# Performance work log

Hardware: AMD Instinct MI355X
Metric: run time of the kernel (lower is better)

## Reference

```python
import jax, jax.numpy as jnp
import numpy as np
import math

B, L = 2048, 60
D, H, NL = 80, 8, 3
HD = D // H            # head_dim = 10
NLOC, NUSR = 1187, 46
DFF = 2 * D
IN_DIM = D + 24 + 32 + 2   # loc(80)+user(24)+weekday(16)+hour(16)+2 continuous


def _ln(x, g, b):
    m = jnp.mean(x, -1, keepdims=True)
    v = jnp.mean((x - m) ** 2, -1, keepdims=True)
    return (x - m) * jax.lax.rsqrt(v + 1e-5) * g + b


def setup_inputs():
    key = jax.random.key(0)
    k = lambda i: jax.random.fold_in(key, i)
    g = lambda i, shp, s: jax.random.normal(k(i), shp, dtype=jnp.float32) * s
    inp = {
        "loc_seq": jax.random.randint(k(0), (B, L), 0, NLOC),
        "user_seq": jax.random.randint(k(1), (B, L), 0, NUSR),
        "weekday_seq": jax.random.randint(k(2), (B, L), 0, 8),
        "start_min_seq": jax.random.randint(k(3), (B, L), 0, 1440),
        "dur_seq": jax.random.randint(k(4), (B, L), 0, 600),
        "diff_seq": jax.random.randint(k(5), (B, L), 0, 100),
        "seq_len": jax.random.randint(k(6), (B,), 1, L + 1),
    }
    # embedding tables (padding_idx=0 rows zeroed where the module uses it)
    inp["loc_table"] = g(10, (NLOC, D), 0.02).at[0].set(0.0)
    inp["user_table"] = g(11, (NUSR, 24), 0.02).at[0].set(0.0)
    inp["wk_table"] = g(12, (8, 16), 0.02).at[0].set(0.0)
    inp["hr_table"] = g(13, (25, 16), 0.02)
    inp["in_w"] = g(14, (IN_DIM, D), 0.09)
    inp["in_b"] = jnp.zeros((D,), jnp.float32)
    inp["in_g"] = jnp.ones((D,), jnp.float32)
    inp["in_be"] = jnp.zeros((D,), jnp.float32)
    inp["pos_emb"] = g(15, (1, L, D), 0.02)
    # per-layer stacked params (NL=3 layers)
    inp["qkv_w"] = g(16, (NL, D, 3 * D), 0.09)
    inp["proj_w"] = g(17, (NL, D, D), 0.11)
    inp["proj_b"] = jnp.zeros((NL, D), jnp.float32)
    inp["rel_emb"] = g(18, (NL, 2 * L - 1, HD), 1.0)
    inp["n1_g"] = jnp.ones((NL, D), jnp.float32)
    inp["n1_b"] = jnp.zeros((NL, D), jnp.float32)
    inp["ffn_w1"] = g(19, (NL, D, DFF), 0.09)
    inp["ffn_b1"] = jnp.zeros((NL, DFF), jnp.float32)
    inp["ffn_w2"] = g(20, (NL, DFF, D), 0.09)
    inp["ffn_b2"] = jnp.zeros((NL, D), jnp.float32)
    inp["n2_g"] = jnp.ones((NL, D), jnp.float32)
    inp["n2_b"] = jnp.zeros((NL, D), jnp.float32)
    inp["fn_g"] = jnp.ones((D,), jnp.float32)
    inp["fn_b"] = jnp.zeros((D,), jnp.float32)
    inp["pr_w1"] = g(21, (D, D), 0.11)
    inp["pr_b1"] = jnp.zeros((D,), jnp.float32)
    inp["pr_w2"] = g(22, (D, NLOC), 0.04)
    inp["pr_b2"] = jnp.zeros((NLOC,), jnp.float32)
    inp["protos"] = g(23, (NLOC, D), 0.04)
    inp["temp"] = jnp.asarray(2.0, jnp.float32)
    return inp


def reference(loc_seq, user_seq, weekday_seq, start_min_seq, dur_seq, diff_seq, seq_len,
              loc_table, user_table, wk_table, hr_table, in_w, in_b, in_g, in_be, pos_emb,
              qkv_w, proj_w, proj_b, rel_emb, n1_g, n1_b, ffn_w1, ffn_b1, ffn_w2, ffn_b2,
              n2_g, n2_b, fn_g, fn_b, pr_w1, pr_b1, pr_w2, pr_b2, protos, temp):
    Bx, Lx = loc_seq.shape
    loc_e = loc_table[loc_seq]                                            # [B,L,80]
    user_e = jnp.broadcast_to(user_table[user_seq[:, 0]][:, None, :], (Bx, Lx, 24))
    hour = jnp.clip(start_min_seq // 60, 0, 23)
    cont = jnp.stack([diff_seq.astype(jnp.float32) / 10.0,
                      dur_seq.astype(jnp.float32) / 300.0], -1)           # [B,L,2]
    x = jnp.concatenate([loc_e, user_e, wk_table[weekday_seq], hr_table[hour], cont], -1)
    x = _ln(x @ in_w + in_b, in_g, in_be) + pos_emb[:, :Lx, :]
    key_mask = loc_seq == 0                                               # mask keys [B,L]
    pos_idx = jnp.arange(Lx)[None, :] - jnp.arange(Lx)[:, None] + (Lx - 1)  # [L,L]
    scale = 1.0 / math.sqrt(HD)
    for l in range(NL):
        qkv = (x @ qkv_w[l]).reshape(Bx, Lx, 3, H, HD)
        q = qkv[:, :, 0].transpose(0, 2, 1, 3)                            # [B,H,L,hd]
        kk = qkv[:, :, 1].transpose(0, 2, 1, 3)
        v = qkv[:, :, 2].transpose(0, 2, 1, 3)
        rel = rel_emb[l][pos_idx]                                         # [L,L,hd]
        attn = (jnp.einsum('bhid,bhjd->bhij', q, kk)
                + jnp.einsum('bhid,ijd->bhij', q, rel)) * scale
        attn = jnp.where(key_mask[:, None, None, :], -jnp.inf, attn)
        a = jax.nn.softmax(attn, -1)
        o = jnp.einsum('bhij,bhjd->bhid', a, v).transpose(0, 2, 1, 3).reshape(Bx, Lx, D)
        x = _ln(x + o @ proj_w[l] + proj_b[l], n1_g[l], n1_b[l])
        f = jax.nn.gelu(x @ ffn_w1[l] + ffn_b1[l], approximate=False) @ ffn_w2[l] + ffn_b2[l]
        x = _ln(x + f, n2_g[l], n2_b[l])
    x = _ln(x, fn_g, fn_b)
    final = x[jnp.arange(Bx), jnp.clip(seq_len - 1, 0, Lx - 1)]           # [B,80]
    logits_param = jax.nn.gelu(final @ pr_w1 + pr_b1, approximate=False) @ pr_w2 + pr_b2
    fnorm = final / jnp.maximum(jnp.linalg.norm(final, axis=-1, keepdims=True), 1e-12)
    pnorm = protos / jnp.maximum(jnp.linalg.norm(protos, axis=-1, keepdims=True), 1e-12)
    logits = 0.5 * logits_param + 0.5 * (fnorm @ pnorm.T) * 15.0
    return logits / jnp.clip(temp, 0.5, 3.0)
```

## Files before the change

kernel.cpp:

```cpp
#include <hip/hip_runtime.h>
#include <hip/hip_bf16.h>
#include <math.h>

#define BB   2048
#define LL   60
#define DD   80
#define HH   8
#define HDD  10
#define NLNUM 3
#define NLOC 1187
#define DFF  160
#define IN_DIM 138
#define RELN 119
#define SCS  68
#define XP   21
#define HP   41
#define VP   35
#define TS   65

__device__ __forceinline__ float gelu_f(float a) {
  float x = fabsf(a) * 0.70710678118654752f;
  float t = 1.0f / (1.0f + 0.3275911f * x);
  float y = t * (0.254829592f + t * (-0.284496736f + t * (1.421413741f +
            t * (-1.453152027f + t * 1.061405429f))));
  float e = 1.0f - y * __expf(-x * x);
  float erf_s = copysignf(e, a);
  return 0.5f * a * (1.0f + erf_s);
}

__global__ __launch_bounds__(256) void k_rprep(
    const float* __restrict__ rel_emb, float* __restrict__ relTg) {
  int idx = blockIdx.x * 256 + threadIdx.x;
  if (idx >= 3600) return;
  int p = idx % 120;
  int d = (idx / 120) % 10;
  int l = idx / 1200;
  float v = 0.0f;
  if (p < RELN) v = rel_emb[l * RELN * HDD + p * HDD + d];
  relTg[idx] = v;
}

__global__ __launch_bounds__(256) void k_embed(
    const int* __restrict__ loc_seq, const int* __restrict__ user_seq,
    const int* __restrict__ wk_seq, const int* __restrict__ sm_seq,
    const int* __restrict__ dur_seq, const int* __restrict__ diff_seq,
    const float* __restrict__ loc_table, const float* __restrict__ user_table,
    const float* __restrict__ wk_table, const float* __restrict__ hr_table,
    const float* __restrict__ in_w, const float* __restrict__ in_b,
    const float* __restrict__ in_g, const float* __restrict__ in_be,
    const float* __restrict__ pos_emb, float* __restrict__ x) {
  int tok0 = blockIdx.x * 48, tid = threadIdx.x;
  __shared__ __align__(16) float vin[48 * VP * 4];
  __shared__ __align__(16) float ws[140 * 80];
  __shared__ float mstd[96];

  float4* vin4 = (float4*)vin;
  float4* ws4  = (float4*)ws;

  for (int i = tid; i < 140 * 20; i += 256) {
    int r = i / 20, c = i % 20;
    float4 v = make_float4(0.0f, 0.0f, 0.0f, 0.0f);
    if (r < IN_DIM) v = *(const float4*)(in_w + r * 80 + c * 4);
    ws4[i] = v;
  }
  for (int i = tid; i < 48 * 35; i += 256) {
    int t = i / 35, s = i % 35;
    int tok = tok0 + t;
    float4 v;
    if (s < 20) {
      int loc = loc_seq[tok];
      v = *(const float4*)(loc_table + (size_t)loc * 80 + s * 4);
    } else if (s < 26) {
      int usr = user_seq[(tok / LL) * LL];
      v = *(const float4*)(user_table + usr * 24 + (s - 20) * 4);
    } else if (s < 30) {
      int wk = wk_seq[tok];
      v = *(const float4*)(wk_table + wk * 16 + (s - 26) * 4);
    } else if (s < 34) {
      int hr = sm_seq[tok] / 60; hr = min(max(hr, 0), 23);
      v = *(const float4*)(hr_table + hr * 16 + (s - 30) * 4);
    } else {
      v.x = (float)diff_seq[tok] / 10.0f;
      v.y = (float)dur_seq[tok] / 300.0f;
      v.z = 0.0f; v.w = 0.0f;
    }
    vin4[t * VP + s] = v;
  }
  __syncthreads();

  int tg = tid / 20, cg = tid % 20, t0 = tg * 4;
  float acc[4][4] = {};
  if (tid < 240) {
    #pragma unroll 7
    for (int iq = 0; iq < 35; iq++) {
      float4 xv[4], wv[4];
      #pragma unroll
      for (int dt = 0; dt < 4; dt++) xv[dt] = vin4[(t0 + dt) * VP + iq];
      #pragma unroll
      for (int di = 0; di < 4; di++) wv[di] = ws4[(iq * 4 + di) * 20 + cg];
      #pragma unroll
      for (int dt = 0; dt < 4; dt++) {
        const float* xp = (const float*)&xv[dt];
        #pragma unroll
        for (int di = 0; di < 4; di++) {
          const float* wp = (const float*)&wv[di];
          #pragma unroll
          for (int dc = 0; dc < 4; dc++) acc[dt][dc] += xp[di] * wp[dc];
        }
      }
    }
  }
  __syncthreads();
  if (tid < 240) {
    float4 bb = *(const float4*)(in_b + cg * 4);
    const float* bp = (const float*)&bb;
    #pragma unroll
    for (int dt = 0; dt < 4; dt++) {
      float4 y;
      y.x = acc[dt][0] + bp[0];
      y.y = acc[dt][1] + bp[1];
      y.z = acc[dt][2] + bp[2];
      y.w = acc[dt][3] + bp[3];
      vin4[(t0 + dt) * VP + cg] = y;
    }
  }
  __syncthreads();
  if (tid < 48) {
    float s = 0.0f, s2 = 0.0f;
    #pragma unroll
    for (int iq = 0; iq < 20; iq++) {
      float4 v = vin4[tid * VP + iq];
      s  += v.x + v.y + v.z + v.w;
      s2 += v.x * v.x + v.y * v.y + v.z * v.z + v.w * v.w;
    }
    float mean = s / 80.0f;
    float var  = fmaxf(s2 / 80.0f - mean * mean, 0.0f);
    mstd[tid] = mean; mstd[48 + tid] = rsqrtf(var + 1e-5f);
  }
  __syncthreads();
  for (int e = tid; e < 960; e += 256) {
    int t = e / 20, c4 = e % 20;
    float4 v = vin4[t * VP + c4];
    float4 gg = *(const float4*)(in_g + c4 * 4);
    float4 bb = *(const float4*)(in_be + c4 * 4);
    float4 pe = *(const float4*)(pos_emb + ((tok0 + t) % LL) * 80 + c4 * 4);
    float m = mstd[t], r = mstd[48 + t];
    float4 out;
    out.x = (v.x - m) * r * gg.x + bb.x + pe.x;
    out.y = (v.y - m) * r * gg.y + bb.y + pe.y;
    out.z = (v.z - m) * r * gg.z + bb.z + pe.z;
    out.w = (v.w - m) * r * gg.w + bb.w + pe.w;
    ((float4*)(x + (size_t)tok0 * 80))[e] = out;
  }
}

__global__ __launch_bounds__(256) void k_qkv(
    const float* __restrict__ x, const float* __restrict__ qkv_w,
    float* __restrict__ qkvo) {
  int b = blockIdx.x, tid = threadIdx.x;
  __shared__ __align__(16) float xsT[20 * TS * 4];
  __shared__ __align__(16) float ws[80 * 60];

  const float4* xb4 = (const float4*)(x + (size_t)b * 4800);
  float4* xsT4 = (float4*)xsT;
  float4* ws4  = (float4*)ws;
  for (int i = tid; i < 1200; i += 256) {
    int t = i / 20, iq = i % 20;
    xsT4[iq * TS + t] = xb4[i];
  }

  for (int c0 = 0; c0 < 240; c0 += 60) {
    __syncthreads();
    for (int i = tid; i < 1200; i += 256)
      ws4[i] = *(const float4*)(qkv_w + (i / 15) * 240 + c0 + (i % 15) * 4);
    __syncthreads();
    if (tid < 225) {
      int tg = tid % 15, cg = tid / 15;
      int t0 = tg * 4;
      float acc[4][4] = {};
      #pragma unroll 5
      for (int iq = 0; iq < 20; iq++) {
        float4 xv[4], wv[4];
        #pragma unroll
        for (int dt = 0; dt < 4; dt++) xv[dt] = xsT4[iq * TS + t0 + dt];
        #pragma unroll
        for (int di = 0; di < 4; di++) wv[di] = ws4[(iq * 4 + di) * 15 + cg];
        #pragma unroll
        for (int dt = 0; dt < 4; dt++) {
          const float* xp = (const float*)&xv[dt];
          #pragma unroll
          for (int di = 0; di < 4; di++) {
            const float* wp = (const float*)&wv[di];
            #pragma unroll
            for (int dc = 0; dc < 4; dc++) acc[dt][dc] += xp[di] * wp[dc];
          }
        }
      }
      float* qb = qkvo + (size_t)b * 14400 + (size_t)(c0 + cg * 4) * 60 + t0;
      #pragma unroll
      for (int dc = 0; dc < 4; dc++)
        *(float4*)(qb + dc * 60) =
            make_float4(acc[0][dc], acc[1][dc], acc[2][dc], acc[3][dc]);
    }
  }
}

__global__ __launch_bounds__(256) void k_attn(
    const float* __restrict__ qkvo, const int* __restrict__ loc_seq,
    const float* __restrict__ relTg,
    float* __restrict__ o) {
  int bh = blockIdx.x;
  int b = bh >> 3, h = bh & 7;
  int tid = threadIdx.x;

  __shared__ __align__(16) float qs[HDD * 60];
  __shared__ __align__(16) float ks[HDD * 60];
  __shared__ __align__(16) float vs[HDD * 60];
  __shared__ __align__(16) float relT[HDD * 120];
  __shared__ __align__(16) float sc[60 * SCS];
  __shared__ __align__(16) float rsum[64];
  __shared__ float msk[60];

  const float4* src = (const float4*)(qkvo + (size_t)b * 14400);
  float4* q4 = (float4*)qs; float4* k4 = (float4*)ks; float4* v4 = (float4*)vs;
  for (int i = tid; i < 150; i += 256) {
    q4[i] = src[h * 150 + i];
    k4[i] = src[1200 + h * 150 + i];
    v4[i] = src[2400 + h * 150 + i];
  }
  const float4* rg4 = (const float4*)relTg;
  float4* relT4 = (float4*)relT;
  for (int i = tid; i < 300; i += 256) relT4[i] = rg4[i];
  if (tid < 60) msk[tid] = (loc_seq[b * LL + tid] == 0) ? 1.0f : 0.0f;
  __syncthreads();

  if (tid < 225) {
    int ig = tid / 15, jg = tid % 15;
    int i0 = ig * 4, j0 = jg * 4;
    int w0 = j0 - i0 + 56;
    float acc[4][4] = {};
    #pragma unroll
    for (int d = 0; d < 10; d++) {
      float4 qv = *(const float4*)(qs + d * 60 + i0);
      float4 kv = *(const float4*)(ks + d * 60 + j0);
      float4 rA = *(const float4*)(relT + d * 120 + w0);
      float4 rB = *(const float4*)(relT + d * 120 + w0 + 4);
      float rr[8] = {rA.x, rA.y, rA.z, rA.w, rB.x, rB.y, rB.z, rB.w};
      const float* qp = (const float*)&qv;
      const float* kp = (const float*)&kv;
      #pragma unroll
      for (int di = 0; di < 4; di++)
        #pragma unroll
        for (int dj = 0; dj < 4; dj++)
          acc[di][dj] += qp[di] * (kp[dj] + rr[dj - di + 3]);
    }
    const float scale = 0.31622776601683794f;
    #pragma unroll
    for (int di = 0; di < 4; di++) {
      #pragma unroll
      for (int dj = 0; dj < 4; dj++) {
        float v = acc[di][dj] * scale;
        if (msk[j0 + dj] != 0.0f) v = -1e30f;
        acc[di][dj] = v;
      }
      *(float4*)(sc + (i0 + di) * SCS + j0) =
          make_float4(acc[di][0], acc[di][1], acc[di][2], acc[di][3]);
    }
  }
  __syncthreads();

  if (tid < 60) {
    float* row = sc + tid * SCS;
    int c = (tid >> 3) & 7;
    float m0 = -3.0e38f, m1 = -3.0e38f, m2 = -3.0e38f, m3 = -3.0e38f;
    #pragma unroll
    for (int s = 0; s < 15; s++) {
      int k = c + s; if (k >= 15) k -= 15;
      float4 v = *(const float4*)(row + 4 * k);
      m0 = fmaxf(m0, v.x); m1 = fmaxf(m1, v.y);
      m2 = fmaxf(m2, v.z); m3 = fmaxf(m3, v.w);
    }
    float m = fmaxf(fmaxf(m0, m1), fmaxf(m2, m3));
    float s0 = 0.0f, s1 = 0.0f, s2 = 0.0f, s3 = 0.0f;
    #pragma unroll
    for (int s = 0; s < 15; s++) {
      int k = c + s; if (k >= 15) k -= 15;
      float4 v = *(float4*)(row + 4 * k);
      v.x = __expf(v.x - m); v.y = __expf(v.y - m);
      v.z = __expf(v.z - m); v.w = __expf(v.w - m);
      *(float4*)(row + 4 * k) = v;
      s0 += v.x; s1 += v.y; s2 += v.z; s3 += v.w;
    }
    rsum[tid] = 1.0f / (s0 + s1 + s2 + s3);
  }
  __syncthreads();

  if (tid < 150) {
    int ig = tid / 10, d = tid % 10;
    float acc[4] = {0, 0, 0, 0};
    #pragma unroll 5
    for (int jq = 0; jq < 15; jq++) {
      float4 vv = *(const float4*)(vs + d * 60 + jq * 4);
      #pragma unroll
      for (int di = 0; di < 4; di++) {
        float4 av = *(const float4*)(sc + (ig + 15 * di) * SCS + jq * 4);
        acc[di] += av.x * vv.x + av.y * vv.y + av.z * vv.z + av.w * vv.w;
      }
    }
    #pragma unroll
    for (int di = 0; di < 4; di++) {
      float r = rsum[ig + 15 * di];
      o[((size_t)b * 60 + ig + 15 * di) * 80 + h * 10 + d] = acc[di] * r;
    }
  }
}

__global__ __launch_bounds__(256) void k_pffn(
    const float* __restrict__ o, const float* __restrict__ proj_w,
    const float* __restrict__ proj_b, const float* __restrict__ g1,
    const float* __restrict__ be1,
    const float* __restrict__ w1, const float* __restrict__ b1,
    const float* __restrict__ w2, const float* __restrict__ b2,
    const float* __restrict__ g2, const float* __restrict__ be2,
    float* __restrict__ x) {
  int tok0 = blockIdx.x * 48, tid = threadIdx.x;
  __shared__ __align__(16) float ys[48 * XP * 4];
  __shared__ __align__(16) float hs[48 * HP * 4];
  __shared__ __align__(16) float ws[80 * 80];
  __shared__ float mstd[96];

  float4* ys4 = (float4*)ys;
  float4* hs4 = (float4*)hs;
  float4* os4 = (float4*)hs;
  float4* ws4 = (float4*)ws;

  const float4* ob4 = (const float4*)(o + (size_t)tok0 * 80);
  for (int i = tid; i < 960; i += 256) os4[(i / 20) * XP + (i % 20)] = ob4[i];
  for (int i = tid; i < 1600; i += 256)
    ws4[i] = *(const float4*)(proj_w + (i / 20) * 80 + (i % 20) * 4);
  __syncthreads();

  int tg = tid / 20, cg = tid % 20, t0 = tg * 4;
  {
    float acc[4][4] = {};
    if (tid < 240) {
      #pragma unroll
      for (int iq = 0; iq < 20; iq++) {
        float4 xv[4], wv[4];
        #pragma unroll
        for (int dt = 0; dt < 4; dt++) xv[dt] = os4[(t0 + dt) * XP + iq];
        #pragma unroll
        for (int di = 0; di < 4; di++) wv[di] = ws4[(iq * 4 + di) * 20 + cg];
        #pragma unroll
        for (int dt = 0; dt < 4; dt++) {
          const float* xp = (const float*)&xv[dt];
          #pragma unroll
          for (int di = 0; di < 4; di++) {
            const float* wp = (const float*)&wv[di];
            #pragma unroll
            for (int dc = 0; dc < 4; dc++) acc[dt][dc] += xp[di] * wp[dc];
          }
        }
      }
      float4 pb = *(const float4*)(proj_b + cg * 4);
      const float* pbp = (const float*)&pb;
      #pragma unroll
      for (int dt = 0; dt < 4; dt++) {
        float4 xr = *(const float4*)(x + (size_t)(tok0 + t0 + dt) * 80 + cg * 4);
        const float* xrp = (const float*)&xr;
        float4 out;
        out.x = acc[dt][0] + pbp[0] + xrp[0];
        out.y = acc[dt][1] + pbp[1] + xrp[1];
        out.z = acc[dt][2] + pbp[2] + xrp[2];
        out.w = acc[dt][3] + pbp[3] + xrp[3];
        ys4[(t0 + dt) * XP + cg] = out;
      }
    }
  }
  __syncthreads();
  if (tid < 48) {
    float s = 0.0f, s2 = 0.0f;
    #pragma unroll
    for (int iq = 0; iq < 20; iq++) {
      float4 v = ys4[tid * XP + iq];
      s  += v.x + v.y + v.z + v.w;
      s2 += v.x * v.x + v.y * v.y + v.z * v.z + v.w * v.w;
    }
    float mean = s / 80.0f;
    float var  = fmaxf(s2 / 80.0f - mean * mean, 0.0f);
    mstd[tid] = mean; mstd[48 + tid] = rsqrtf(var + 1e-5f);
  }
  __syncthreads();
  for (int e = tid; e < 960; e += 256) {
    int t = e / 20, c4 = e % 20;
    float4 v = ys4[t * XP + c4];
    float4 gg = *(const float4*)(g1 + c4 * 4);
    float4 bb = *(const float4*)(be1 + c4 * 4);
    float m = mstd[t], r = mstd[48 + t];
    v.x = (v.x - m) * r * gg.x + bb.x;
    v.y = (v.y - m) * r * gg.y + bb.y;
    v.z = (v.z - m) * r * gg.z + bb.z;
    v.w = (v.w - m) * r * gg.w + bb.w;
    ys4[t * XP + c4] = v;
  }

  for (int c0 = 0; c0 < 160; c0 += 80) {
    __syncthreads();
    for (int i = tid; i < 1600; i += 256)
      ws4[i] = *(const float4*)(w1 + (i / 20) * 160 + c0 + (i % 20) * 4);
    __syncthreads();
    if (tid < 240) {
      float acc[4][4] = {};
      #pragma unroll
      for (int iq = 0; iq < 20; iq++) {
        float4 xv[4], wv[4];
        #pragma unroll
        for (int dt = 0; dt < 4; dt++) xv[dt] = ys4[(t0 + dt) * XP + iq];
        #pragma unroll
        for (int di = 0; di < 4; di++) wv[di] = ws4[(iq * 4 + di) * 20 + cg];
        #pragma unroll
        for (int dt = 0; dt < 4; dt++) {
          const float* xp = (const float*)&xv[dt];
          #pragma unroll
          for (int di = 0; di < 4; di++) {
            const float* wp = (const float*)&wv[di];
            #pragma unroll
            for (int dc = 0; dc < 4; dc++) acc[dt][dc] += xp[di] * wp[dc];
          }
        }
      }
      float4 bb = *(const float4*)(b1 + c0 + cg * 4);
      const float* bp = (const float*)&bb;
      #pragma unroll
      for (int dt = 0; dt < 4; dt++) {
        float4 out;
        float* op = (float*)&out;
        #pragma unroll
        for (int dc = 0; dc < 4; dc++)
          op[dc] = gelu_f(acc[dt][dc] + bp[dc]);
        hs4[(t0 + dt) * HP + c0 / 4 + cg] = out;
      }
    }
  }

  float acc[4][4] = {};
  for (int k0 = 0; k0 < 160; k0 += 80) {
    __syncthreads();
    for (int i = tid; i < 1600; i += 256)
      ws4[i] = *(const float4*)(w2 + (size_t)(k0 + i / 20) * 80 + (i % 20) * 4);
    __syncthreads();
    if (tid < 240) {
      #pragma unroll
      for (int iq = 0; iq < 20; iq++) {
        float4 hv[4], wv[4];
        #pragma unroll
        for (int dt = 0; dt < 4; dt++) hv[dt] = hs4[(t0 + dt) * HP + k0 / 4 + iq];
        #pragma unroll
        for (int di = 0; di < 4; di++) wv[di] = ws4[(iq * 4 + di) * 20 + cg];
        #pragma unroll
        for (int dt = 0; dt < 4; dt++) {
          const float* hp = (const float*)&hv[dt];
          #pragma unroll
          for (int di = 0; di < 4; di++) {
            const float* wp = (const float*)&wv[di];
            #pragma unroll
            for (int dc = 0; dc < 4; dc++) acc[dt][dc] += hp[di] * wp[dc];
          }
        }
      }
    }
  }
  __syncthreads();
  if (tid < 240) {
    float4 bb = *(const float4*)(b2 + cg * 4);
    const float* bp = (const float*)&bb;
    #pragma unroll
    for (int dt = 0; dt < 4; dt++) {
      float4 xr = ys4[(t0 + dt) * XP + cg];
      const float* xrp = (const float*)&xr;
      float4 out;
      out.x = acc[dt][0] + bp[0] + xrp[0];
      out.y = acc[dt][1] + bp[1] + xrp[1];
      out.z = acc[dt][2] + bp[2] + xrp[2];
      out.w = acc[dt][3] + bp[3] + xrp[3];
      hs4[(t0 + dt) * HP + cg] = out;
    }
  }
  __syncthreads();
  if (tid < 48) {
    float s = 0.0f, s2 = 0.0f;
    #pragma unroll
    for (int iq = 0; iq < 20; iq++) {
      float4 v = hs4[tid * HP + iq];
      s  += v.x + v.y + v.z + v.w;
      s2 += v.x * v.x + v.y * v.y + v.z * v.z + v.w * v.w;
    }
    float mean = s / 80.0f;
    float var  = fmaxf(s2 / 80.0f - mean * mean, 0.0f);
    mstd[tid] = mean; mstd[48 + tid] = rsqrtf(var + 1e-5f);
  }
  __syncthreads();
  for (int e = tid; e < 960; e += 256) {
    int t = e / 20, c4 = e % 20;
    float4 v = hs4[t * HP + c4];
    float4 gg = *(const float4*)(g2 + c4 * 4);
    float4 bb = *(const float4*)(be2 + c4 * 4);
    float m = mstd[t], r = mstd[48 + t];
    float4 out;
    out.x = (v.x - m) * r * gg.x + bb.x;
    out.y = (v.y - m) * r * gg.y + bb.y;
    out.z = (v.z - m) * r * gg.z + bb.z;
    out.w = (v.w - m) * r * gg.w + bb.w;
    ((float4*)(x + (size_t)tok0 * 80))[e] = out;
  }
}

__global__ __launch_bounds__(128) void k_final(
    const float* __restrict__ x, const int* __restrict__ seq_len,
    const float* __restrict__ fn_g, const float* __restrict__ fn_b,
    const float* __restrict__ pr_w1, const float* __restrict__ pr_b1,
    float* __restrict__ fnorm, float* __restrict__ h1) {
  int b = blockIdx.x, tid = threadIdx.x;
  __shared__ float red[128], red2[128];
  __shared__ float fbuf[DD];
  int t = seq_len[b] - 1; t = min(max(t, 0), LL - 1);
  float v = 0.0f;
  if (tid < DD) v = x[((size_t)b * LL + t) * DD + tid];
  red[tid]  = (tid < DD) ? v : 0.0f;
  red2[tid] = (tid < DD) ? v * v : 0.0f;
  __syncthreads();
  for (int s = 64; s > 0; s >>= 1) {
    if (tid < s) { red[tid] += red[tid + s]; red2[tid] += red2[tid + s]; }
    __syncthreads();
  }
  float mean = red[0] / DD;
  float var  = fmaxf(red2[0] / DD - mean * mean, 0.0f);
  float rstd = rsqrtf(var + 1e-5f);
  float f = 0.0f;
  if (tid < DD) { f = (v - mean) * rstd * fn_g[tid] + fn_b[tid]; fbuf[tid] = f; }
  __syncthreads();
  red[tid] = (tid < DD) ? f * f : 0.0f;
  __syncthreads();
  for (int s = 64; s > 0; s >>= 1) {
    if (tid < s) red[tid] += red[tid + s];
    __syncthreads();
  }
  float rn = 1.0f / fmaxf(sqrtf(red[0]), 1e-12f);
  if (tid < DD) {
    fnorm[(size_t)b * DD + tid] = f * rn;
    float gacc = pr_b1[tid];
    for (int i = 0; i < DD; i++) gacc += fbuf[i] * pr_w1[i * DD + tid];
    h1[(size_t)b * DD + tid] = gelu_f(gacc);
  }
}

__global__ __launch_bounds__(128) void k_pnorm(
    const float* __restrict__ protos, float* __restrict__ pnormT) {
  int c = blockIdx.x, tid = threadIdx.x;
  __shared__ float red[128];
  float v = 0.0f;
  if (tid < DD) v = protos[(size_t)c * DD + tid];
  red[tid] = (tid < DD) ? v * v : 0.0f;
  __syncthreads();
  for (int s = 64; s > 0; s >>= 1) {
    if (tid < s) red[tid] += red[tid + s];
    __syncthreads();
  }
  float rn = 1.0f / fmaxf(sqrtf(red[0]), 1e-12f);
  if (tid < DD) pnormT[(size_t)tid * NLOC + c] = v * rn;
}

__global__ __launch_bounds__(256) void k_logits(
    const float* __restrict__ h1, const float* __restrict__ fnorm,
    const float* __restrict__ pr_w2, const float* __restrict__ pr_b2,
    const float* __restrict__ pnormT, const float* __restrict__ temp,
    float* __restrict__ out) {
  int b0 = (blockIdx.x / 5) * 4, cb = blockIdx.x % 5;
  int tid = threadIdx.x;
  int c = cb * 256 + tid;
  __shared__ float h1s[4][DD], fns[4][DD];
  for (int i = tid; i < 4 * DD; i += 256) {
    int j = i / DD, k = i % DD;
    h1s[j][k] = h1[(size_t)(b0 + j) * DD + k];
    fns[j][k] = fnorm[(size_t)(b0 + j) * DD + k];
  }
  __syncthreads();
  if (c < NLOC) {
    float a1[4] = {0, 0, 0, 0}, a2[4] = {0, 0, 0, 0};
    for (int k = 0; k < DD; k++) {
      float w = pr_w2[(size_t)k * NLOC + c];
      float p = pnormT[(size_t)k * NLOC + c];
      #pragma unroll
      for (int j = 0; j < 4; j++) {
        a1[j] += h1s[j][k] * w;
        a2[j] += fns[j][k] * p;
      }
    }
    float pb = pr_b2[c];
    float tt = fminf(fmaxf(temp[0], 0.5f), 3.0f);
    #pragma unroll
    for (int j = 0; j < 4; j++)
      out[(size_t)(b0 + j) * NLOC + c] = (0.5f * (a1[j] + pb) + 7.5f * a2[j]) / tt;
  }
}

extern "C" void kernel_launch(void* const* d_in, const int* in_sizes, int n_in,
                              void* d_out, int out_size, void* d_ws, size_t ws_size,
                              hipStream_t stream) {
  const int* loc_seq   = (const int*)d_in[0];
  const int* user_seq  = (const int*)d_in[1];
  const int* wk_seq    = (const int*)d_in[2];
  const int* sm_seq    = (const int*)d_in[3];
  const int* dur_seq   = (const int*)d_in[4];
  const int* diff_seq  = (const int*)d_in[5];
  const int* seq_len   = (const int*)d_in[6];
  const float* loc_table = (const float*)d_in[7];
  const float* user_table= (const float*)d_in[8];
  const float* wk_table  = (const float*)d_in[9];
  const float* hr_table  = (const float*)d_in[10];
  const float* in_w   = (const float*)d_in[11];
  const float* in_b   = (const float*)d_in[12];
  const float* in_g   = (const float*)d_in[13];
  const float* in_be  = (const float*)d_in[14];
  const float* pos_emb= (const float*)d_in[15];
  const float* qkv_w  = (const float*)d_in[16];
  const float* proj_w = (const float*)d_in[17];
  const float* proj_b = (const float*)d_in[18];
  const float* rel_emb= (const float*)d_in[19];
  const float* n1_g   = (const float*)d_in[20];
  const float* n1_b   = (const float*)d_in[21];
  const float* ffn_w1 = (const float*)d_in[22];
  const float* ffn_b1 = (const float*)d_in[23];
  const float* ffn_w2 = (const float*)d_in[24];
  const float* ffn_b2 = (const float*)d_in[25];
  const float* n2_g   = (const float*)d_in[26];
  const float* n2_b   = (const float*)d_in[27];
  const float* fn_g   = (const float*)d_in[28];
  const float* fn_b   = (const float*)d_in[29];
  const float* pr_w1  = (const float*)d_in[30];
  const float* pr_b1  = (const float*)d_in[31];
  const float* pr_w2  = (const float*)d_in[32];
  const float* pr_b2  = (const float*)d_in[33];
  const float* protos = (const float*)d_in[34];
  const float* temp   = (const float*)d_in[35];
  float* out = (float*)d_out;

  float* x      = (float*)d_ws;
  float* o      = x + (size_t)BB * LL * DD;
  float* qkvo   = o + (size_t)BB * LL * DD;
  float* fnorm  = qkvo + (size_t)BB * 14400;
  float* h1     = fnorm + (size_t)BB * DD;
  float* pnormT = h1 + (size_t)BB * DD;
  float* relTg  = pnormT + (size_t)DD * NLOC;

  k_rprep<<<15, 256, 0, stream>>>(rel_emb, relTg);

  k_embed<<<BB * LL / 48, 256, 0, stream>>>(loc_seq, user_seq, wk_seq, sm_seq,
                                            dur_seq, diff_seq, loc_table,
                                            user_table, wk_table, hr_table,
                                            in_w, in_b, in_g, in_be, pos_emb, x);

  for (int l = 0; l < NLNUM; l++) {
    k_qkv<<<BB, 256, 0, stream>>>(x, qkv_w + (size_t)l * 80 * 240, qkvo);
    k_attn<<<BB * HH, 256, 0, stream>>>(qkvo, loc_seq,
                                        relTg + (size_t)l * 1200, o);
    k_pffn<<<BB * LL / 48, 256, 0, stream>>>(
        o, proj_w + (size_t)l * DD * DD, proj_b + (size_t)l * DD,
        n1_g + (size_t)l * DD, n1_b + (size_t)l * DD,
        ffn_w1 + (size_t)l * DD * DFF, ffn_b1 + (size_t)l * DFF,
        ffn_w2 + (size_t)l * DFF * DD, ffn_b2 + (size_t)l * DD,
        n2_g + (size_t)l * DD, n2_b + (size_t)l * DD, x);
  }

  k_pnorm<<<NLOC, 128, 0, stream>>>(protos, pnormT);
  k_final<<<BB, 128, 0, stream>>>(x, seq_len, fn_g, fn_b, pr_w1, pr_b1, fnorm, h1);
  k_logits<<<(BB / 4) * 5, 256, 0, stream>>>(h1, fnorm, pr_w2, pr_b2, pnormT, temp, out);
}
```

Before: 1.520 ms.

## Chunk weight staging in embed and proj/FFN kernels to shrink shared memory

The embed kernel now stages the input projection weights in two chunks instead of holding the full 140x80 matrix in shared memory. The proj+FFN kernel splits the projection and FFN1 outputs into column chunks and fuses FFN1 with FFN2 per hidden chunk. This removes the full 160-wide hidden buffer and halves the weight tile. The aim is lower LDS use per block so more blocks fit per CU, at the cost of extra barriers and smaller per-thread tiles (2x4 instead of 4x4) in some phases.

```diff
diff --git a/kernel.cpp b/kernel.cpp
--- a/kernel.cpp
+++ b/kernel.cpp
@@ -14,7 +14,7 @@
 #define RELN 119
 #define SCS  68
 #define XP   21
-#define HP   41
+#define HP2  11
 #define VP   35
 #define TS   65
 
@@ -51,18 +51,12 @@
     const float* __restrict__ pos_emb, float* __restrict__ x) {
   int tok0 = blockIdx.x * 48, tid = threadIdx.x;
   __shared__ __align__(16) float vin[48 * VP * 4];
-  __shared__ __align__(16) float ws[140 * 80];
+  __shared__ __align__(16) float ws[1440 * 4];
   __shared__ float mstd[96];
 
   float4* vin4 = (float4*)vin;
   float4* ws4  = (float4*)ws;
 
-  for (int i = tid; i < 140 * 20; i += 256) {
-    int r = i / 20, c = i % 20;
-    float4 v = make_float4(0.0f, 0.0f, 0.0f, 0.0f);
-    if (r < IN_DIM) v = *(const float4*)(in_w + r * 80 + c * 4);
-    ws4[i] = v;
-  }
   for (int i = tid; i < 48 * 35; i += 256) {
     int t = i / 35, s = i % 35;
     int tok = tok0 + t;
@@ -86,31 +80,40 @@
     }
     vin4[t * VP + s] = v;
   }
-  __syncthreads();
 
   int tg = tid / 20, cg = tid % 20, t0 = tg * 4;
   float acc[4][4] = {};
-  if (tid < 240) {
-    #pragma unroll 7
-    for (int iq = 0; iq < 35; iq++) {
-      float4 xv[4], wv[4];
-      #pragma unroll
-      for (int dt = 0; dt < 4; dt++) xv[dt] = vin4[(t0 + dt) * VP + iq];
-      #pragma unroll
-      for (int di = 0; di < 4; di++) wv[di] = ws4[(iq * 4 + di) * 20 + cg];
-      #pragma unroll
-      for (int dt = 0; dt < 4; dt++) {
-        const float* xp = (const float*)&xv[dt];
-        #pragma unroll
-        for (int di = 0; di < 4; di++) {
-          const float* wp = (const float*)&wv[di];
+  for (int cc = 0; cc < 2; cc++) {
+    int iq0 = cc * 18, niq = cc ? 17 : 18;
+    for (int i = tid; i < niq * 80; i += 256) {
+      int r = i / 20, c = i % 20;
+      int grow = iq0 * 4 + r;
+      float4 v = make_float4(0.0f, 0.0f, 0.0f, 0.0f);
+      if (grow < IN_DIM) v = *(const float4*)(in_w + grow * 80 + c * 4);
+      ws4[r * 20 + c] = v;
+    }
+    __syncthreads();
+    if (tid < 240) {
+      for (int iq = 0; iq < niq; iq++) {
+        float4 xv[4], wv[4];
+        #pragma unroll
+        for (int dt = 0; dt < 4; dt++) xv[dt] = vin4[(t0 + dt) * VP + iq0 + iq];
+        #pragma unroll
+        for (int di = 0; di < 4; di++) wv[di] = ws4[(iq * 4 + di) * 20 + cg];
+        #pragma unroll
+        for (int dt = 0; dt < 4; dt++) {
+          const float* xp = (const float*)&xv[dt];
           #pragma unroll
-          for (int dc = 0; dc < 4; dc++) acc[dt][dc] += xp[di] * wp[dc];
+          for (int di = 0; di < 4; di++) {
+            const float* wp = (const float*)&wv[di];
+            #pragma unroll
+            for (int dc = 0; dc < 4; dc++) acc[dt][dc] += xp[di] * wp[dc];
+          }
         }
       }
     }
-  }
-  __syncthreads();
+    __syncthreads();
+  }
   if (tid < 240) {
     float4 bb = *(const float4*)(in_b + cg * 4);
     const float* bp = (const float*)&bb;
@@ -325,34 +328,37 @@
     float* __restrict__ x) {
   int tok0 = blockIdx.x * 48, tid = threadIdx.x;
   __shared__ __align__(16) float ys[48 * XP * 4];
-  __shared__ __align__(16) float hs[48 * HP * 4];
-  __shared__ __align__(16) float ws[80 * 80];
+  __shared__ __align__(16) float oh[48 * XP * 4];
+  __shared__ __align__(16) float ws[800 * 4];
   __shared__ float mstd[96];
 
   float4* ys4 = (float4*)ys;
-  float4* hs4 = (float4*)hs;
-  float4* os4 = (float4*)hs;
+  float4* oh4 = (float4*)oh;
   float4* ws4 = (float4*)ws;
+  const float4* pw4 = (const float4*)proj_w;
+  const float4* w14 = (const float4*)w1;
+  const float4* w24 = (const float4*)w2;
+
+  int tgA = tid / 10, cgA = tid % 10, t0A = tgA * 2;
+  int tgC = tid / 20, cgC = tid % 20, t0C = tgC * 4;
 
   const float4* ob4 = (const float4*)(o + (size_t)tok0 * 80);
-  for (int i = tid; i < 960; i += 256) os4[(i / 20) * XP + (i % 20)] = ob4[i];
-  for (int i = tid; i < 1600; i += 256)
-    ws4[i] = *(const float4*)(proj_w + (i / 20) * 80 + (i % 20) * 4);
-  __syncthreads();
-
-  int tg = tid / 20, cg = tid % 20, t0 = tg * 4;
-  {
-    float acc[4][4] = {};
+  for (int i = tid; i < 960; i += 256) oh4[(i / 20) * XP + (i % 20)] = ob4[i];
+  for (int cc = 0; cc < 2; cc++) {
+    for (int i = tid; i < 800; i += 256)
+      ws4[i] = pw4[(i / 10) * 20 + cc * 10 + (i % 10)];
+    __syncthreads();
     if (tid < 240) {
-      #pragma unroll
+      float acc[2][4] = {};
+      #pragma unroll 5
       for (int iq = 0; iq < 20; iq++) {
-        float4 xv[4], wv[4];
-        #pragma unroll
-        for (int dt = 0; dt < 4; dt++) xv[dt] = os4[(t0 + dt) * XP + iq];
-        #pragma unroll
-        for (int di = 0; di < 4; di++) wv[di] = ws4[(iq * 4 + di) * 20 + cg];
-        #pragma unroll
-        for (int dt = 0; dt < 4; dt++) {
+        float4 xv[2], wv[4];
+        #pragma unroll
+        for (int dt = 0; dt < 2; dt++) xv[dt] = oh4[(t0A + dt) * XP + iq];
+        #pragma unroll
+        for (int di = 0; di < 4; di++) wv[di] = ws4[(iq * 4 + di) * 10 + cgA];
+        #pragma unroll
+        for (int dt = 0; dt < 2; dt++) {
           const float* xp = (const float*)&xv[dt];
           #pragma unroll
           for (int di = 0; di < 4; di++) {
@@ -362,22 +368,23 @@
           }
         }
       }
-      float4 pb = *(const float4*)(proj_b + cg * 4);
+      float4 pb = ((const float4*)proj_b)[cc * 10 + cgA];
       const float* pbp = (const float*)&pb;
       #pragma unroll
-      for (int dt = 0; dt < 4; dt++) {
-        float4 xr = *(const float4*)(x + (size_t)(tok0 + t0 + dt) * 80 + cg * 4);
+      for (int dt = 0; dt < 2; dt++) {
+        float4 xr = *(const float4*)(x + (size_t)(tok0 + t0A + dt) * 80 +
+                                     (cc * 10 + cgA) * 4);
         const float* xrp = (const float*)&xr;
         float4 out;
         out.x = acc[dt][0] + pbp[0] + xrp[0];
         out.y = acc[dt][1] + pbp[1] + xrp[1];
         out.z = acc[dt][2] + pbp[2] + xrp[2];
         out.w = acc[dt][3] + pbp[3] + xrp[3];
-        ys4[(t0 + dt) * XP + cg] = out;
-      }
-    }
-  }
-  __syncthreads();
+        ys4[(t0A + dt) * XP + cc * 10 + cgA] = out;
+      }
+    }
+    __syncthreads();
+  }
   if (tid < 48) {
     float s = 0.0f, s2 = 0.0f;
     #pragma unroll
@@ -404,22 +411,22 @@
     ys4[t * XP + c4] = v;
   }
 
-  for (int c0 = 0; c0 < 160; c0 += 80) {
-    __syncthreads();
-    for (int i = tid; i < 1600; i += 256)
-      ws4[i] = *(const float4*)(w1 + (i / 20) * 160 + c0 + (i % 20) * 4);
+  float accC[4][4] = {};
+  for (int hc = 0; hc < 4; hc++) {
+    for (int i = tid; i < 800; i += 256)
+      ws4[i] = w14[(i / 10) * 40 + hc * 10 + (i % 10)];
     __syncthreads();
     if (tid < 240) {
-      float acc[4][4] = {};
-      #pragma unroll
+      float acc[2][4] = {};
+      #pragma unroll 5
       for (int iq = 0; iq < 20; iq++) {
-        float4 xv[4], wv[4];
-        #pragma unroll
-        for (int dt = 0; dt < 4; dt++) xv[dt] = ys4[(t0 + dt) * XP + iq];
-        #pragma unroll
-        for (int di = 0; di < 4; di++) wv[di] = ws4[(iq * 4 + di) * 20 + cg];
-        #pragma unroll
-        for (int dt = 0; dt < 4; dt++) {
+        float4 xv[2], wv[4];
+        #pragma unroll
+        for (int dt = 0; dt < 2; dt++) xv[dt] = ys4[(t0A + dt) * XP + iq];
+        #pragma unroll
+        for (int di = 0; di < 4; di++) wv[di] = ws4[(iq * 4 + di) * 10 + cgA];
+        #pragma unroll
+        for (int dt = 0; dt < 2; dt++) {
           const float* xp = (const float*)&xv[dt];
           #pragma unroll
           for (int di = 0; di < 4; di++) {
@@ -429,34 +436,30 @@
           }
         }
       }
-      float4 bb = *(const float4*)(b1 + c0 + cg * 4);
+      float4 bb = ((const float4*)b1)[hc * 10 + cgA];
       const float* bp = (const float*)&bb;
       #pragma unroll
-      for (int dt = 0; dt < 4; dt++) {
-        float4 out;
-        float* op = (float*)&out;
-        #pragma unroll
-        for (int dc = 0; dc < 4; dc++)
-          op[dc] = gelu_f(acc[dt][dc] + bp[dc]);
-        hs4[(t0 + dt) * HP + c0 / 4 + cg] = out;
-      }
-    }
-  }
-
-  float acc[4][4] = {};
-  for (int k0 = 0; k0 < 160; k0 += 80) {
-    __syncthreads();
-    for (int i = tid; i < 1600; i += 256)
-      ws4[i] = *(const float4*)(w2 + (size_t)(k0 + i / 20) * 80 + (i % 20) * 4);
+      for (int dt = 0; dt < 2; dt++) {
+        float4 hv;
+        hv.x = gelu_f(acc[dt][0] + bp[0]);
+        hv.y = gelu_f(acc[dt][1] + bp[1]);
+        hv.z = gelu_f(acc[dt][2] + bp[2]);
+        hv.w = gelu_f(acc[dt][3] + bp[3]);
+        oh4[(t0A + dt) * HP2 + cgA] = hv;
+      }
+    }
+    __syncthreads();
+    for (int i = tid; i < 800; i += 256)
+      ws4[i] = w24[(hc * 40 + i / 20) * 20 + (i % 20)];
     __syncthreads();
     if (tid < 240) {
-      #pragma unroll
-      for (int iq = 0; iq < 20; iq++) {
+      #pragma unroll 5
+      for (int iq = 0; iq < 10; iq++) {
         float4 hv[4], wv[4];
         #pragma unroll
-        for (int dt = 0; dt < 4; dt++) hv[dt] = hs4[(t0 + dt) * HP + k0 / 4 + iq];
-        #pragma unroll
-        for (int di = 0; di < 4; di++) wv[di] = ws4[(iq * 4 + di) * 20 + cg];
+        for (int dt = 0; dt < 4; dt++) hv[dt] = oh4[(t0C + dt) * HP2 + iq];
+        #pragma unroll
+        for (int di = 0; di < 4; di++) wv[di] = ws4[(iq * 4 + di) * 20 + cgC];
         #pragma unroll
         for (int dt = 0; dt < 4; dt++) {
           const float* hp = (const float*)&hv[dt];
@@ -464,26 +467,27 @@
           for (int di = 0; di < 4; di++) {
             const float* wp = (const float*)&wv[di];
             #pragma unroll
-            for (int dc = 0; dc < 4; dc++) acc[dt][dc] += hp[di] * wp[dc];
+            for (int dc = 0; dc < 4; dc++) accC[dt][dc] += hp[di] * wp[dc];
           }
         }
       }
     }
-  }
-  __syncthreads();
+    __syncthreads();
+  }
+
   if (tid < 240) {
-    float4 bb = *(const float4*)(b2 + cg * 4);
+    float4 bb = ((const float4*)b2)[cgC];
     const float* bp = (const float*)&bb;
     #pragma unroll
     for (int dt = 0; dt < 4; dt++) {
-      float4 xr = ys4[(t0 + dt) * XP + cg];
-      const float* xrp = (const float*)&xr;
+      float4 yv = ys4[(t0C + dt) * XP + cgC];
+      const float* yp = (const float*)&yv;
       float4 out;
-      out.x = acc[dt][0] + bp[0] + xrp[0];
-      out.y = acc[dt][1] + bp[1] + xrp[1];
-      out.z = acc[dt][2] + bp[2] + xrp[2];
-      out.w = acc[dt][3] + bp[3] + xrp[3];
-      hs4[(t0 + dt) * HP + cg] = out;
+      out.x = accC[dt][0] + bp[0] + yp[0];
+      out.y = accC[dt][1] + bp[1] + yp[1];
+      out.z = accC[dt][2] + bp[2] + yp[2];
+      out.w = accC[dt][3] + bp[3] + yp[3];
+      oh4[(t0C + dt) * XP + cgC] = out;
     }
   }
   __syncthreads();
@@ -491,7 +495,7 @@
     float s = 0.0f, s2 = 0.0f;
     #pragma unroll
     for (int iq = 0; iq < 20; iq++) {
-      float4 v = hs4[tid * HP + iq];
+      float4 v = oh4[tid * XP + iq];
       s  += v.x + v.y + v.z + v.w;
       s2 += v.x * v.x + v.y * v.y + v.z * v.z + v.w * v.w;
     }
@@ -502,7 +506,7 @@
   __syncthreads();
   for (int e = tid; e < 960; e += 256) {
     int t = e / 20, c4 = e % 20;
-    float4 v = hs4[t * HP + c4];
+    float4 v = oh4[t * XP + c4];
     float4 gg = *(const float4*)(g2 + c4 * 4);
     float4 bb = *(const float4*)(be2 + c4 * 4);
     float m = mstd[t], r = mstd[48 + t];
```

Measured after the change: 1.579 ms. 1.04x slower.

## Fuse QKV projection and attention into one kernel per batch-half

Applied to the files above, without the earlier changes.

Merges the QKV projection and attention kernels so that each block computes Q/K/V for four heads of one sequence straight into shared memory and then runs attention over those heads. This removes the global qkvo write and re-read and one kernel launch per layer. In exchange, the block count drops from 16384 to 4096, the attention steps for the four heads run one after another inside each block, and shared memory rises to about 68KB per block, which may lower occupancy. The x tile is also loaded twice per sequence, once by each head-half block.

```diff
diff --git a/kernel.cpp b/kernel.cpp
--- a/kernel.cpp
+++ b/kernel.cpp
@@ -154,12 +154,24 @@
   }
 }
 
-__global__ __launch_bounds__(256) void k_qkv(
+__global__ __launch_bounds__(256) void k_qkvattn(
     const float* __restrict__ x, const float* __restrict__ qkv_w,
-    float* __restrict__ qkvo) {
-  int b = blockIdx.x, tid = threadIdx.x;
-  __shared__ __align__(16) float xsT[20 * TS * 4];
-  __shared__ __align__(16) float ws[80 * 60];
+    const int* __restrict__ loc_seq,
+    const float* __restrict__ relTg,
+    float* __restrict__ o) {
+  int blk = blockIdx.x;
+  int b = blk >> 1;
+  int h0 = (blk & 1) * 4;
+  int tid = threadIdx.x;
+
+  __shared__ __align__(16) float qkvs[120 * 60];
+  __shared__ __align__(16) float U[10000];
+  float* xsT = U;
+  float* ws  = U + 5200;
+  float* sc   = U;
+  float* relT = U + 4080;
+  float* rsum = U + 5280;
+  float* msk  = U + 5344;
 
   const float4* xb4 = (const float4*)(x + (size_t)b * 4800);
   float4* xsT4 = (float4*)xsT;
@@ -168,11 +180,18 @@
     int t = i / 20, iq = i % 20;
     xsT4[iq * TS + t] = xb4[i];
   }
-
-  for (int c0 = 0; c0 < 240; c0 += 60) {
-    __syncthreads();
-    for (int i = tid; i < 1200; i += 256)
-      ws4[i] = *(const float4*)(qkv_w + (i / 15) * 240 + c0 + (i % 15) * 4);
+  int qb4 = (h0 >> 1) * 5;
+  const float4* qw4 = (const float4*)qkv_w;
+  for (int pass = 0; pass < 2; pass++) {
+    __syncthreads();
+    for (int i = tid; i < 1200; i += 256) {
+      int r = i / 15, f = i % 15;
+      int cl4 = pass * 15 + f;
+      int g4 = (cl4 < 10) ? (qb4 + cl4)
+             : (cl4 < 20) ? (20 + qb4 + (cl4 - 10))
+                          : (40 + qb4 + (cl4 - 20));
+      ws4[i] = qw4[r * 60 + g4];
+    }
     __syncthreads();
     if (tid < 225) {
       int tg = tid % 15, cg = tid / 15;
@@ -196,122 +215,107 @@
           }
         }
       }
-      float* qb = qkvo + (size_t)b * 14400 + (size_t)(c0 + cg * 4) * 60 + t0;
+      float* qb = qkvs + (pass * 60 + cg * 4) * 60 + t0;
       #pragma unroll
       for (int dc = 0; dc < 4; dc++)
         *(float4*)(qb + dc * 60) =
             make_float4(acc[0][dc], acc[1][dc], acc[2][dc], acc[3][dc]);
     }
   }
-}
-
-__global__ __launch_bounds__(256) void k_attn(
-    const float* __restrict__ qkvo, const int* __restrict__ loc_seq,
-    const float* __restrict__ relTg,
-    float* __restrict__ o) {
-  int bh = blockIdx.x;
-  int b = bh >> 3, h = bh & 7;
-  int tid = threadIdx.x;
-
-  __shared__ __align__(16) float qs[HDD * 60];
-  __shared__ __align__(16) float ks[HDD * 60];
-  __shared__ __align__(16) float vs[HDD * 60];
-  __shared__ __align__(16) float relT[HDD * 120];
-  __shared__ __align__(16) float sc[60 * SCS];
-  __shared__ __align__(16) float rsum[64];
-  __shared__ float msk[60];
-
-  const float4* src = (const float4*)(qkvo + (size_t)b * 14400);
-  float4* q4 = (float4*)qs; float4* k4 = (float4*)ks; float4* v4 = (float4*)vs;
-  for (int i = tid; i < 150; i += 256) {
-    q4[i] = src[h * 150 + i];
-    k4[i] = src[1200 + h * 150 + i];
-    v4[i] = src[2400 + h * 150 + i];
-  }
+  __syncthreads();
+
   const float4* rg4 = (const float4*)relTg;
   float4* relT4 = (float4*)relT;
   for (int i = tid; i < 300; i += 256) relT4[i] = rg4[i];
   if (tid < 60) msk[tid] = (loc_seq[b * LL + tid] == 0) ? 1.0f : 0.0f;
   __syncthreads();
 
-  if (tid < 225) {
-    int ig = tid / 15, jg = tid % 15;
-    int i0 = ig * 4, j0 = jg * 4;
-    int w0 = j0 - i0 + 56;
-    float acc[4][4] = {};
-    #pragma unroll
-    for (int d = 0; d < 10; d++) {
-      float4 qv = *(const float4*)(qs + d * 60 + i0);
-      float4 kv = *(const float4*)(ks + d * 60 + j0);
-      float4 rA = *(const float4*)(relT + d * 120 + w0);
-      float4 rB = *(const float4*)(relT + d * 120 + w0 + 4);
-      float rr[8] = {rA.x, rA.y, rA.z, rA.w, rB.x, rB.y, rB.z, rB.w};
-      const float* qp = (const float*)&qv;
-      const float* kp = (const float*)&kv;
-      #pragma unroll
-      for (int di = 0; di < 4; di++)
-        #pragma unroll
-        for (int dj = 0; dj < 4; dj++)
-          acc[di][dj] += qp[di] * (kp[dj] + rr[dj - di + 3]);
-    }
-    const float scale = 0.31622776601683794f;
-    #pragma unroll
-    for (int di = 0; di < 4; di++) {
-      #pragma unroll
-      for (int dj = 0; dj < 4; dj++) {
-        float v = acc[di][dj] * scale;
-        if (msk[j0 + dj] != 0.0f) v = -1e30f;
-        acc[di][dj] = v;
-      }
-      *(float4*)(sc + (i0 + di) * SCS + j0) =
-          make_float4(acc[di][0], acc[di][1], acc[di][2], acc[di][3]);
-    }
-  }
-  __syncthreads();
-
-  if (tid < 60) {
-    float* row = sc + tid * SCS;
-    int c = (tid >> 3) & 7;
-    float m0 = -3.0e38f, m1 = -3.0e38f, m2 = -3.0e38f, m3 = -3.0e38f;
-    #pragma unroll
-    for (int s = 0; s < 15; s++) {
-      int k = c + s; if (k >= 15) k -= 15;
-      float4 v = *(const float4*)(row + 4 * k);
-      m0 = fmaxf(m0, v.x); m1 = fmaxf(m1, v.y);
-      m2 = fmaxf(m2, v.z); m3 = fmaxf(m3, v.w);
-    }
-    float m = fmaxf(fmaxf(m0, m1), fmaxf(m2, m3));
-    float s0 = 0.0f, s1 = 0.0f, s2 = 0.0f, s3 = 0.0f;
-    #pragma unroll
-    for (int s = 0; s < 15; s++) {
-      int k = c + s; if (k >= 15) k -= 15;
-      float4 v = *(float4*)(row + 4 * k);
-      v.x = __expf(v.x - m); v.y = __expf(v.y - m);
-      v.z = __expf(v.z - m); v.w = __expf(v.w - m);
-      *(float4*)(row + 4 * k) = v;
-      s0 += v.x; s1 += v.y; s2 += v.z; s3 += v.w;
-    }
-    rsum[tid] = 1.0f / (s0 + s1 + s2 + s3);
-  }
-  __syncthreads();
-
-  if (tid < 150) {
-    int ig = tid / 10, d = tid % 10;
-    float acc[4] = {0, 0, 0, 0};
-    #pragma unroll 5
-    for (int jq = 0; jq < 15; jq++) {
-      float4 vv = *(const float4*)(vs + d * 60 + jq * 4);
+  for (int hh = 0; hh < 4; hh++) {
+    const float* qs = qkvs + hh * 600;
+    const float* ks = qkvs + 2400 + hh * 600;
+    const float* vs = qkvs + 4800 + hh * 600;
+    int h = h0 + hh;
+
+    if (tid < 225) {
+      int ig = tid / 15, jg = tid % 15;
+      int i0 = ig * 4, j0 = jg * 4;
+      int w0 = j0 - i0 + 56;
+      float acc[4][4] = {};
+      #pragma unroll
+      for (int d = 0; d < 10; d++) {
+        float4 qv = *(const float4*)(qs + d * 60 + i0);
+        float4 kv = *(const float4*)(ks + d * 60 + j0);
+        float4 rA = *(const float4*)(relT + d * 120 + w0);
+        float4 rB = *(const float4*)(relT + d * 120 + w0 + 4);
+        float rr[8] = {rA.x, rA.y, rA.z, rA.w, rB.x, rB.y, rB.z, rB.w};
+        const float* qp = (const float*)&qv;
+        const float* kp = (const float*)&kv;
+        #pragma unroll
+        for (int di = 0; di < 4; di++)
+          #pragma unroll
+          for (int dj = 0; dj < 4; dj++)
+            acc[di][dj] += qp[di] * (kp[dj] + rr[dj - di + 3]);
+      }
+      const float scale = 0.31622776601683794f;
       #pragma unroll
       for (int di = 0; di < 4; di++) {
-        float4 av = *(const float4*)(sc + (ig + 15 * di) * SCS + jq * 4);
-        acc[di] += av.x * vv.x + av.y * vv.y + av.z * vv.z + av.w * vv.w;
-      }
-    }
-    #pragma unroll
-    for (int di = 0; di < 4; di++) {
-      float r = rsum[ig + 15 * di];
-      o[((size_t)b * 60 + ig + 15 * di) * 80 + h * 10 + d] = acc[di] * r;
-    }
+        #pragma unroll
+        for (int dj = 0; dj < 4; dj++) {
+          float v = acc[di][dj] * scale;
+          if (msk[j0 + dj] != 0.0f) v = -1e30f;
+          acc[di][dj] = v;
+        }
+        *(float4*)(sc + (i0 + di) * SCS + j0) =
+            make_float4(acc[di][0], acc[di][1], acc[di][2], acc[di][3]);
+      }
+    }
+    __syncthreads();
+
+    if (tid < 60) {
+      float* row = sc + tid * SCS;
+      int c = (tid >> 3) & 7;
+      float m0 = -3.0e38f, m1 = -3.0e38f, m2 = -3.0e38f, m3 = -3.0e38f;
+      #pragma unroll
+      for (int s = 0; s < 15; s++) {
+        int k = c + s; if (k >= 15) k -= 15;
+        float4 v = *(const float4*)(row + 4 * k);
+        m0 = fmaxf(m0, v.x); m1 = fmaxf(m1, v.y);
+        m2 = fmaxf(m2, v.z); m3 = fmaxf(m3, v.w);
+      }
+      float m = fmaxf(fmaxf(m0, m1), fmaxf(m2, m3));
+      float s0 = 0.0f, s1 = 0.0f, s2 = 0.0f, s3 = 0.0f;
+      #pragma unroll
+      for (int s = 0; s < 15; s++) {
+        int k = c + s; if (k >= 15) k -= 15;
+        float4 v = *(float4*)(row + 4 * k);
+        v.x = __expf(v.x - m); v.y = __expf(v.y - m);
+        v.z = __expf(v.z - m); v.w = __expf(v.w - m);
+        *(float4*)(row + 4 * k) = v;
+        s0 += v.x; s1 += v.y; s2 += v.z; s3 += v.w;
+      }
+      rsum[tid] = 1.0f / (s0 + s1 + s2 + s3);
+    }
+    __syncthreads();
+
+    if (tid < 150) {
+      int ig = tid / 10, d = tid % 10;
+      float acc[4] = {0, 0, 0, 0};
+      #pragma unroll 5
+      for (int jq = 0; jq < 15; jq++) {
+        float4 vv = *(const float4*)(vs + d * 60 + jq * 4);
+        #pragma unroll
+        for (int di = 0; di < 4; di++) {
+          float4 av = *(const float4*)(sc + (ig + 15 * di) * SCS + jq * 4);
+          acc[di] += av.x * vv.x + av.y * vv.y + av.z * vv.z + av.w * vv.w;
+        }
+      }
+      #pragma unroll
+      for (int di = 0; di < 4; di++) {
+        float r = rsum[ig + 15 * di];
+        o[((size_t)b * 60 + ig + 15 * di) * 80 + h * 10 + d] = acc[di] * r;
+      }
+    }
+    __syncthreads();
   }
 }
 
@@ -661,9 +665,8 @@
                                             in_w, in_b, in_g, in_be, pos_emb, x);
 
   for (int l = 0; l < NLNUM; l++) {
-    k_qkv<<<BB, 256, 0, stream>>>(x, qkv_w + (size_t)l * 80 * 240, qkvo);
-    k_attn<<<BB * HH, 256, 0, stream>>>(qkvo, loc_seq,
-                                        relTg + (size_t)l * 1200, o);
+    k_qkvattn<<<BB * 2, 256, 0, stream>>>(x, qkv_w + (size_t)l * 80 * 240,
+                                          loc_seq, relTg + (size_t)l * 1200, o);
     k_pffn<<<BB * LL / 48, 256, 0, stream>>>(
         o, proj_w + (size_t)l * DD * DD, proj_b + (size_t)l * DD,
         n1_g + (size_t)l * DD, n1_b + (size_t)l * DD,
```

Result: slower. 1.580 ms (+4.0%).
